# Optimization experiments

Hardware: AMD Instinct MI355X
Metric: run time of the kernel (lower is better)

The kernel has to match this reference:

```python
import jax, jax.numpy as jnp
import numpy as np

N, C, H, T, D, K = 4096, 512, 128, 64, 20, 10


def setup_inputs() -> dict:
    key = jax.random.key(0)
    ks = jax.random.split(key, 40)
    s = 0.05
    inp = {}
    inp["x"] = jax.random.normal(ks[0], (N, D * T), jnp.float32)
    inp["concept_matrix"] = (jax.random.uniform(ks[1], (N, C)) < 0.05).astype(jnp.float32)
    inp["market_value"] = jax.random.uniform(ks[2], (N,), jnp.float32) + 0.1
    # GRU params (torch layout: w_ih [3H,in], w_hh [3H,H], biases [3H]); 2 layers
    inp["gru_w_ih0"] = jax.random.normal(ks[3], (3 * H, D), jnp.float32) * s
    inp["gru_w_hh0"] = jax.random.normal(ks[4], (3 * H, H), jnp.float32) * s
    inp["gru_b_ih0"] = jax.random.normal(ks[5], (3 * H,), jnp.float32) * s
    inp["gru_b_hh0"] = jax.random.normal(ks[6], (3 * H,), jnp.float32) * s
    inp["gru_w_ih1"] = jax.random.normal(ks[7], (3 * H, H), jnp.float32) * s
    inp["gru_w_hh1"] = jax.random.normal(ks[8], (3 * H, H), jnp.float32) * s
    inp["gru_b_ih1"] = jax.random.normal(ks[9], (3 * H,), jnp.float32) * s
    inp["gru_b_hh1"] = jax.random.normal(ks[10], (3 * H,), jnp.float32) * s
    names = ["ps", "hs", "ps_fore", "hs_fore", "ps_back", "hs_back", "indi"]
    for i, n in enumerate(names):
        inp["w_" + n] = jax.random.normal(ks[11 + 2 * i], (H, H), jnp.float32) * s
        inp["b_" + n] = jax.random.normal(ks[12 + 2 * i], (H,), jnp.float32) * s
    inp["w_out"] = jax.random.normal(ks[30], (1, H), jnp.float32) * s
    inp["b_out"] = jax.random.normal(ks[31], (1,), jnp.float32) * s
    return inp


def _cos_sim(x, y):
    # x [n,d], y [m,d] -> [n,m]; NaN (0/0) replaced by 0 via safe denominator
    xy = x @ y.T
    nx = jnp.sqrt(jnp.sum(x * x, axis=1))[:, None]
    ny = jnp.sqrt(jnp.sum(y * y, axis=1))[:, None]
    return xy / jnp.maximum(nx @ ny.T, 1e-12)


def _gru_layer(seq, wih, whh, bih, bhh):
    # seq [T, n, in] -> outputs [T, n, H]
    n = seq.shape[1]
    h0 = jnp.zeros((n, whh.shape[1]), seq.dtype)

    def step(h, xt):
        gx = xt @ wih.T + bih
        gh = h @ whh.T + bhh
        gxr, gxz, gxn = jnp.split(gx, 3, axis=1)
        ghr, ghz, ghn = jnp.split(gh, 3, axis=1)
        r = jax.nn.sigmoid(gxr + ghr)
        z = jax.nn.sigmoid(gxz + ghz)
        ncand = jnp.tanh(gxn + r * ghn)
        hnew = (1.0 - z) * ncand + z * h
        return hnew, hnew

    _, out = jax.lax.scan(step, h0, seq)
    return out


def reference(x, concept_matrix, market_value,
              gru_w_ih0, gru_w_hh0, gru_b_ih0, gru_b_hh0,
              gru_w_ih1, gru_w_hh1, gru_b_ih1, gru_b_hh1,
              w_ps, b_ps, w_hs, b_hs, w_ps_fore, b_ps_fore, w_hs_fore, b_hs_fore,
              w_ps_back, b_ps_back, w_hs_back, b_hs_back, w_indi, b_indi,
              w_out, b_out):
    n = x.shape[0]
    # [n, D*T] -> [n, D, T] -> [n, T, D] -> [T, n, D]
    seq = jnp.swapaxes(x.reshape(n, D, -1).transpose(0, 2, 1), 0, 1)
    out0 = _gru_layer(seq, gru_w_ih0, gru_w_hh0, gru_b_ih0, gru_b_hh0)
    out1 = _gru_layer(out0, gru_w_ih1, gru_w_hh1, gru_b_ih1, gru_b_hh1)
    x_hidden = out1[-1]  # [n, H]

    # --- predefined-concept branch ---
    s2c = concept_matrix * market_value[:, None]
    s2c_den = jnp.sum(s2c, axis=0)[None, :] * concept_matrix + 1.0
    s2c = s2c / s2c_den
    hidden = s2c.T @ x_hidden  # [C, H]
    v1 = jnp.sum(hidden, axis=1) != 0  # valid concepts (replaces row filtering)
    s2c2 = jax.nn.softmax(x_hidden @ hidden.T, axis=0)  # [n, C], column-wise
    hidden2 = s2c2.T @ x_hidden  # [C, H]
    c2s = _cos_sim(x_hidden, hidden2)
    c2s = jax.nn.softmax(jnp.where(v1[None, :], c2s, -1e9), axis=1) * v1[None, :]
    p_shared = c2s @ hidden2
    p_shared = p_shared @ w_ps.T + b_ps
    p_back = p_shared @ w_ps_back.T + b_ps_back
    out_ps = jax.nn.leaky_relu(p_shared @ w_ps_fore.T + b_ps_fore)

    # --- hidden-concept branch ---
    h_shared = x_hidden - p_back
    hs2c = _cos_sim(h_shared, h_shared)  # [n, n]
    diag = jnp.diagonal(hs2c)
    hs2c = hs2c * (1.0 - jnp.eye(n, dtype=hs2c.dtype))
    _, idx = jax.lax.top_k(hs2c, K)  # [n, K]
    mask = jnp.zeros_like(hs2c).at[jnp.arange(n)[:, None], idx].set(1.0)
    hs2c = hs2c * mask
    hs2c = hs2c + jnp.diag((jnp.sum(hs2c, axis=0) != 0).astype(hs2c.dtype) * diag)
    hidden_h = (h_shared.T @ hs2c).T  # [n, H]
    v2 = jnp.sum(hidden_h, axis=1) != 0
    hc2s = _cos_sim(h_shared, hidden_h)
    hc2s = jax.nn.softmax(jnp.where(v2[None, :], hc2s, -1e9), axis=1) * v2[None, :]
    h_si = hc2s @ hidden_h
    h_si = h_si @ w_hs.T + b_hs
    h_back = h_si @ w_hs_back.T + b_hs_back
    out_hs = jax.nn.leaky_relu(h_si @ w_hs_fore.T + b_hs_fore)

    # --- individual branch + head ---
    indi = x_hidden - p_back - h_back
    out_indi = jax.nn.leaky_relu(indi @ w_indi.T + b_indi)
    all_info = out_ps + out_hs + out_indi
    return (all_info @ w_out.T + b_out).squeeze()
```

## Files before the change

kernel.cpp:

```cpp
#include <hip/hip_runtime.h>
#include <cstddef>

#define NR 4096
#define CDIM 512
#define HDIM 128
#define TSTEPS 64
#define DDIM 20
#define KTOP 10

typedef __attribute__((ext_vector_type(8))) short short8;
typedef __attribute__((ext_vector_type(4))) float f32x4;

__device__ __forceinline__ unsigned short f2bf(float f) {
    union { float f; unsigned u; } x; x.f = f;
    unsigned r = (x.u + 0x7fffu + ((x.u >> 16) & 1u)) >> 16;
    return (unsigned short)r;
}
__device__ __forceinline__ unsigned short f2bf_t(float f) {
    union { float f; unsigned u; } x; x.f = f;
    return (unsigned short)(x.u >> 16);
}
__device__ __forceinline__ float bf2f(unsigned short h) {
    union { unsigned u; float f; } x; x.u = ((unsigned)h) << 16;
    return x.f;
}
__device__ __forceinline__ float sigm(float v) {
    return __builtin_amdgcn_rcpf(1.f + __expf(-v));
}
__device__ __forceinline__ float tanh_f(float v) {
    return 1.f - 2.f * __builtin_amdgcn_rcpf(1.f + __expf(2.f * v));
}

#define MFMA16(a, b, c) __builtin_amdgcn_mfma_f32_16x16x32_bf16(a, b, c, 0, 0, 0)

struct MG {
    const float* A; const unsigned short* Bh; const unsigned short* Bl;
    const float* bias; float* C; const float* aux; float* sub;
    const unsigned short* Ah; const unsigned short* Al;
    int N, K, kchunk, flags;
};

__global__ __launch_bounds__(256) void mfma_gemm(MG g)
{
    const int tid = threadIdx.x;
    const int w = tid >> 6, lane = tid & 63, quad = lane >> 4, lm = lane & 15;
    const int bm = (blockIdx.y << 6) + (w << 4);
    const int bn = blockIdx.x << 6;
    const int NC = g.K >> 5;
    const int c0 = (blockIdx.z * g.kchunk) >> 5;
    const int c1 = c0 + (g.kchunk >> 5);
    const float* arow = g.A + (size_t)(bm + lm) * g.K;
    const int packA = g.flags & 16;
    f32x4 acc[4];
    #pragma unroll
    for (int t = 0; t < 4; t++) acc[t] = (f32x4){0.f, 0.f, 0.f, 0.f};

    for (int c = c0; c < c1; c++) {
        short8 ah, al;
        if (packA) {
            size_t aidx = ((size_t)((bm >> 4) * NC + c) * 64 + lane) * 8;
            ah = *(const short8*)(g.Ah + aidx);
            al = *(const short8*)(g.Al + aidx);
        } else {
            const float* ap = arow + (c << 5) + (quad << 3);
            float4 a0 = *(const float4*)ap;
            float4 a1 = *(const float4*)(ap + 4);
            #pragma unroll
            for (int jj = 0; jj < 4; jj++) {
                float f = (&a0.x)[jj];
                unsigned short h = f2bf(f);
                ah[jj] = h; al[jj] = f2bf_t(f - bf2f(h));
                f = (&a1.x)[jj];
                h = f2bf(f);
                ah[4 + jj] = h; al[4 + jj] = f2bf_t(f - bf2f(h));
            }
        }
        #pragma unroll
        for (int t = 0; t < 4; t++) {
            size_t bidx = ((size_t)(((bn >> 4) + t) * NC + c) * 64 + lane) * 8;
            short8 bh = *(const short8*)(g.Bh + bidx);
            short8 bl = *(const short8*)(g.Bl + bidx);
            acc[t] = MFMA16(ah, bh, acc[t]);
            acc[t] = MFMA16(ah, bl, acc[t]);
            acc[t] = MFMA16(al, bh, acc[t]);
        }
    }
    #pragma unroll
    for (int t = 0; t < 4; t++) {
        #pragma unroll
        for (int rg = 0; rg < 4; rg++) {
            int row = bm + (quad << 2) + rg;
            int col = bn + (t << 4) + lm;
            float v = acc[t][rg];
            if (g.flags & 1) v += g.bias[col];
            if (g.flags & 2) v = v > 0.f ? v : 0.01f * v;
            if (g.flags & 4) atomicAdd(&g.C[(size_t)row * g.N + col], v);
            else g.C[(size_t)row * g.N + col] = v;
            if (g.flags & 8)
                g.sub[(size_t)row * g.N + col] = g.aux[(size_t)row * g.N + col] - v;
        }
    }
}

__global__ void pack_bt(const float* __restrict__ src, unsigned short* __restrict__ hi,
                        unsigned short* __restrict__ lo, int K, int total)
{
    int idx = blockIdx.x * 256 + threadIdx.x;
    if (idx >= total) return;
    int NC = K >> 5;
    int lane = idx & 63;
    int c = (idx >> 6) % NC;
    int t = idx / (NC * 64);
    int n = (t << 4) + (lane & 15);
    int kb = (c << 5) + ((lane >> 4) << 3);
    #pragma unroll
    for (int j = 0; j < 8; j++) {
        float f = src[(size_t)n * K + kb + j];
        unsigned short h = f2bf(f);
        hi[(size_t)idx * 8 + j] = h;
        lo[(size_t)idx * 8 + j] = f2bf_t(f - bf2f(h));
    }
}

__global__ void pack_both(const float* __restrict__ src,
                          unsigned short* __restrict__ bth, unsigned short* __restrict__ btl,
                          unsigned short* __restrict__ knh, unsigned short* __restrict__ knl,
                          int N, int total_kn)
{
    int idx = blockIdx.x * 256 + threadIdx.x;
    int lane = idx & 63;
    int totBT = (N >> 4) * 256;
    if (idx < totBT) {
        int c = (idx >> 6) & 3;
        int t = idx >> 8;
        int n = (t << 4) + (lane & 15);
        int kb = (c << 5) + ((lane >> 4) << 3);
        #pragma unroll
        for (int j = 0; j < 8; j++) {
            float f = src[(size_t)n * HDIM + kb + j];
            unsigned short h = f2bf(f);
            bth[(size_t)idx * 8 + j] = h;
            btl[(size_t)idx * 8 + j] = f2bf_t(f - bf2f(h));
        }
    }
    if (idx < total_kn) {
        int NC = N >> 5;
        int c = (idx >> 6) % NC;
        int t = idx / (NC * 64);
        int n = (t << 4) + (lane & 15);
        int kb = (c << 5) + ((lane >> 4) << 3);
        #pragma unroll
        for (int j = 0; j < 8; j++) {
            float f = src[(size_t)(kb + j) * HDIM + n];
            unsigned short h = f2bf(f);
            knh[(size_t)idx * 8 + j] = h;
            knl[(size_t)idx * 8 + j] = f2bf_t(f - bf2f(h));
        }
    }
}

struct W7 {
    const float* src[7];
    unsigned short* hi[7];
    unsigned short* lo[7];
};
__global__ void pack_w7(W7 p)
{
    int idx = blockIdx.x * 256 + threadIdx.x;
    if (idx >= 7 * 2048) return;
    int m = idx >> 11;
    int r = idx & 2047;
    int lane = r & 63;
    int c = (r >> 6) & 3;
    int t = r >> 8;
    int n = (t << 4) + (lane & 15);
    int kb = (c << 5) + ((lane >> 4) << 3);
    const float* src = p.src[m];
    unsigned short* hi = p.hi[m];
    unsigned short* lo = p.lo[m];
    #pragma unroll
    for (int j = 0; j < 8; j++) {
        float f = src[(size_t)n * HDIM + kb + j];
        unsigned short h = f2bf(f);
        hi[(size_t)r * 8 + j] = h;
        lo[(size_t)r * 8 + j] = f2bf_t(f - bf2f(h));
    }
}

__global__ __launch_bounds__(256) void scan_topk(const float* __restrict__ S,
        const float* __restrict__ hn, float* __restrict__ diagv,
        float* __restrict__ tvals, int* __restrict__ tidx)
{
    int row = blockIdx.x;
    const float* d = S + (size_t)row * NR;
    int tid = threadIdx.x;
    int wv = tid >> 6, lane = tid & 63;
    float hi_ = hn[row];
    float lv[16];
    #pragma unroll
    for (int i = 0; i < 16; i++) {
        int j = tid + (i << 8);
        float v = d[j] / fmaxf(hi_ * hn[j], 1e-12f);
        if (j == row) { diagv[row] = v; v = 0.f; }
        lv[i] = v;
    }
    __shared__ float sv[4];
    __shared__ int si[4];
    for (int k = 0; k < KTOP; k++) {
        float bv = -INFINITY; int bi = 0x7fffffff;
        #pragma unroll
        for (int i = 0; i < 16; i++) {
            int j = tid + (i << 8);
            if (lv[i] > bv || (lv[i] == bv && j < bi)) { bv = lv[i]; bi = j; }
        }
        #pragma unroll
        for (int m = 1; m < 64; m <<= 1) {
            float ov = __shfl_xor(bv, m); int oi = __shfl_xor(bi, m);
            if (ov > bv || (ov == bv && oi < bi)) { bv = ov; bi = oi; }
        }
        if (lane == 0) { sv[wv] = bv; si[wv] = bi; }
        __syncthreads();
        bv = sv[0]; bi = si[0];
        #pragma unroll
        for (int w = 1; w < 4; w++) {
            float ov = sv[w]; int oi = si[w];
            if (ov > bv || (ov == bv && oi < bi)) { bv = ov; bi = oi; }
        }
        if (tid == 0) { tvals[row * KTOP + k] = bv; tidx[row * KTOP + k] = bi; }
        if ((bi & 255) == tid) lv[bi >> 8] = -INFINITY;
        __syncthreads();
    }
}

__global__ __launch_bounds__(512) void hc2s_flash(
    const float* __restrict__ hsh, const float* __restrict__ hn,
    const float* __restrict__ hhn, const float* __restrict__ v2,
    const unsigned short* __restrict__ Bh, const unsigned short* __restrict__ Bl,
    const unsigned short* __restrict__ Vh, const unsigned short* __restrict__ Vl,
    float* __restrict__ pO, float* __restrict__ pM, float* __restrict__ pL)
{
    __shared__ __attribute__((aligned(16))) unsigned short Ph[8][16 * 72];
    __shared__ __attribute__((aligned(16))) unsigned short Plo[8][16 * 72];

    const int tid = threadIdx.x;
    const int wv = tid >> 6, lane = tid & 63, quad = lane >> 4, lm = lane & 15;
    const int rg2 = wv >> 1;
    const int cc = wv & 1;
    const int bm = (blockIdx.x << 6) + (rg2 << 4);
    const int rgg = (blockIdx.x << 2) + rg2;
    const int pidx = (blockIdx.y << 1) + cc;
    const int jt0 = (blockIdx.y << 4) + (cc << 3);

    short8 ahh[4], ahl[4];
    #pragma unroll
    for (int c = 0; c < 4; c++) {
        const float* ap = hsh + (size_t)(bm + lm) * HDIM + (c << 5) + (quad << 3);
        float4 a0 = *(const float4*)ap;
        float4 a1 = *(const float4*)(ap + 4);
        #pragma unroll
        for (int j = 0; j < 4; j++) {
            float f = (&a0.x)[j];
            unsigned short h = f2bf(f);
            ahh[c][j] = h; ahl[c][j] = f2bf_t(f - bf2f(h));
            f = (&a1.x)[j];
            h = f2bf(f);
            ahh[c][4 + j] = h; ahl[c][4 + j] = f2bf_t(f - bf2f(h));
        }
    }
    float hnr[4];
    #pragma unroll
    for (int rg = 0; rg < 4; rg++) hnr[rg] = hn[bm + (quad << 2) + rg];

    float m_old[4], l_old[4];
    #pragma unroll
    for (int rg = 0; rg < 4; rg++) { m_old[rg] = -INFINITY; l_old[rg] = 0.f; }
    f32x4 o[8];
    #pragma unroll
    for (int vt = 0; vt < 8; vt++) o[vt] = (f32x4){0.f, 0.f, 0.f, 0.f};

    const int pwr = lm * 72;
    for (int it = 0; it < 8; it++) {
        const int jt = jt0 + it;
        f32x4 s[4];
        #pragma unroll
        for (int tg = 0; tg < 4; tg++) {
            s[tg] = (f32x4){0.f, 0.f, 0.f, 0.f};
            #pragma unroll
            for (int c = 0; c < 4; c++) {
                size_t bidx = ((size_t)(((jt << 2) + tg) * 4 + c) * 64 + lane) * 8;
                short8 bh = *(const short8*)(Bh + bidx);
                short8 bl = *(const short8*)(Bl + bidx);
                s[tg] = MFMA16(ahh[c], bh, s[tg]);
                s[tg] = MFMA16(ahh[c], bl, s[tg]);
                s[tg] = MFMA16(ahl[c], bh, s[tg]);
            }
        }
        float sv[4][4];
        #pragma unroll
        for (int tg = 0; tg < 4; tg++) {
            int col = (jt << 6) + (tg << 4) + lm;
            float hc = hhn[col];
            float vm = v2[col];
            #pragma unroll
            for (int rg = 0; rg < 4; rg++) {
                float v = s[tg][rg] * __builtin_amdgcn_rcpf(fmaxf(hnr[rg] * hc, 1e-12f));
                sv[tg][rg] = (vm == 0.f) ? -1e9f : v;
            }
        }
        float m_new[4], alpha[4], tsum[4], pv[4][4];
        #pragma unroll
        for (int rg = 0; rg < 4; rg++) {
            float m = fmaxf(fmaxf(sv[0][rg], sv[1][rg]), fmaxf(sv[2][rg], sv[3][rg]));
            #pragma unroll
            for (int d = 1; d < 16; d <<= 1) m = fmaxf(m, __shfl_xor(m, d));
            m_new[rg] = fmaxf(m_old[rg], m);
            alpha[rg] = __expf(m_old[rg] - m_new[rg]);
        }
        #pragma unroll
        for (int rg = 0; rg < 4; rg++) {
            float p0_ = __expf(sv[0][rg] - m_new[rg]);
            float p1_ = __expf(sv[1][rg] - m_new[rg]);
            float p2_ = __expf(sv[2][rg] - m_new[rg]);
            float p3_ = __expf(sv[3][rg] - m_new[rg]);
            pv[0][rg] = p0_; pv[1][rg] = p1_; pv[2][rg] = p2_; pv[3][rg] = p3_;
            float ss = p0_ + p1_ + p2_ + p3_;
            #pragma unroll
            for (int d = 1; d < 16; d <<= 1) ss += __shfl_xor(ss, d);
            tsum[rg] = ss;
        }
        #pragma unroll
        for (int rg = 0; rg < 4; rg++) {
            l_old[rg] = l_old[rg] * alpha[rg] + tsum[rg];
            m_old[rg] = m_new[rg];
        }
        #pragma unroll
        for (int vt = 0; vt < 8; vt++) {
            #pragma unroll
            for (int rg = 0; rg < 4; rg++) o[vt][rg] *= alpha[rg];
        }
        #pragma unroll
        for (int tg = 0; tg < 4; tg++) {
            #pragma unroll
            for (int rg = 0; rg < 4; rg++) {
                int off = ((quad << 2) + rg) * 72 + (tg << 4) + lm;
                float p = pv[tg][rg];
                unsigned short h = f2bf(p);
                Ph[wv][off] = h;
                Plo[wv][off] = f2bf_t(p - bf2f(h));
            }
        }
        __asm__ volatile("s_waitcnt lgkmcnt(0)" ::: "memory");
        #pragma unroll
        for (int c2 = 0; c2 < 2; c2++) {
            int poff = pwr + (c2 << 5) + (quad << 3);
            short8 pah = *(const short8*)&Ph[wv][poff];
            short8 pal = *(const short8*)&Plo[wv][poff];
            int cg = (jt << 1) + c2;
            #pragma unroll
            for (int vt = 0; vt < 8; vt++) {
                size_t b0 = ((size_t)(vt * 128 + cg) * 64 + lane) * 8;
                short8 vh = *(const short8*)(Vh + b0);
                short8 vl = *(const short8*)(Vl + b0);
                o[vt] = MFMA16(pah, vh, o[vt]);
                o[vt] = MFMA16(pah, vl, o[vt]);
                o[vt] = MFMA16(pal, vh, o[vt]);
            }
        }
    }
    size_t pb = ((size_t)rgg * 8 + pidx) * 16;
    #pragma unroll
    for (int rg = 0; rg < 4; rg++) {
        int r = (quad << 2) + rg;
        #pragma unroll
        for (int vt = 0; vt < 8; vt++)
            pO[(pb + r) * 128 + (vt << 4) + lm] = o[vt][rg];
    }
    if (lm == 0) {
        #pragma unroll
        for (int rg = 0; rg < 4; rg++) {
            int r = (quad << 2) + rg;
            pM[pb + r] = m_old[rg];
            pL[pb + r] = l_old[rg];
        }
    }
}

__global__ __launch_bounds__(256) void hc2s_merge(const float* __restrict__ pO,
        const float* __restrict__ pM, const float* __restrict__ pL,
        float* __restrict__ O)
{
    int rgg = blockIdx.x;
    int tid = threadIdx.x;
    int r = tid >> 4;
    int c0 = (tid & 15) << 3;
    float m[8], e[8];
    float M = -INFINITY;
    #pragma unroll
    for (int i = 0; i < 8; i++) {
        m[i] = pM[((size_t)rgg * 8 + i) * 16 + r];
        M = fmaxf(M, m[i]);
    }
    float L = 0.f;
    #pragma unroll
    for (int i = 0; i < 8; i++) {
        e[i] = __expf(m[i] - M);
        L += pL[((size_t)rgg * 8 + i) * 16 + r] * e[i];
    }
    float invL = __builtin_amdgcn_rcpf(L);
    float a[8];
    #pragma unroll
    for (int k = 0; k < 8; k++) a[k] = 0.f;
    #pragma unroll
    for (int i = 0; i < 8; i++) {
        const float* src = pO + (((size_t)rgg * 8 + i) * 16 + r) * 128 + c0;
        float4 v0 = *(const float4*)src;
        float4 v1 = *(const float4*)(src + 4);
        a[0] += v0.x * e[i]; a[1] += v0.y * e[i]; a[2] += v0.z * e[i]; a[3] += v0.w * e[i];
        a[4] += v1.x * e[i]; a[5] += v1.y * e[i]; a[6] += v1.z * e[i]; a[7] += v1.w * e[i];
    }
    float* dst = O + ((size_t)rgg * 16 + r) * 128 + c0;
    #pragma unroll
    for (int k = 0; k < 8; k++) dst[k] = a[k] * invL;
}

__global__ void pack_wb(const float* __restrict__ W, unsigned short* __restrict__ Wp,
                        int K, int nch)
{
    int idx = blockIdx.x * 256 + threadIdx.x;
    if (idx >= 24 * nch * 64) return;
    int lane = idx & 63;
    int c = (idx >> 6) % nch;
    int t = idx / (nch * 64);
    int n = t * 16 + (lane & 15);
    int kb = c * 32 + (lane >> 4) * 8;
    #pragma unroll
    for (int j = 0; j < 8; j++) {
        int k = kb + j;
        float f = (k < K) ? W[(size_t)n * K + k] : 0.f;
        Wp[(size_t)idx * 8 + j] = f2bf(f);
    }
}

__global__ __launch_bounds__(512, 2) void gru_mfma(
    const float* __restrict__ xg,
    const unsigned short* __restrict__ wih0p,
    const unsigned short* __restrict__ whh0p,
    const unsigned short* __restrict__ wih1p,
    const unsigned short* __restrict__ whh1p,
    const float* __restrict__ bih0, const float* __restrict__ bhh0,
    const float* __restrict__ bih1, const float* __restrict__ bhh1,
    float* __restrict__ xh)
{
    __shared__ __attribute__((aligned(16))) unsigned short h0A[2][2][16 * 136];
    __shared__ __attribute__((aligned(16))) unsigned short h1A[2][2][16 * 136];
    __shared__ __attribute__((aligned(16))) unsigned short xA[2][2][16 * 40];

    const int tid = threadIdx.x;
    const int w2 = tid >> 6;
    const int lane = tid & 63;
    const int quad = lane >> 4;
    const int lm = lane & 15;
    const int n0 = blockIdx.x << 4;
    const int j = (w2 << 4) + lm;

    for (int i = tid; i < 2 * 2 * 16 * 136; i += 512) {
        ((unsigned short*)h0A)[i] = 0;
        ((unsigned short*)h1A)[i] = 0;
    }
    for (int i = tid; i < 2 * 2 * 16 * 40; i += 512) ((unsigned short*)xA)[i] = 0;

    float br0 = bih0[j] + bhh0[j];
    float bz0 = bih0[128 + j] + bhh0[128 + j];
    float bni0 = bih0[256 + j];
    float bnh0 = bhh0[256 + j];
    float br1 = bih1[j] + bhh1[j];
    float bz1 = bih1[128 + j] + bhh1[128 + j];
    float bni1 = bih1[256 + j];
    float bnh1 = bhh1[256 + j];

    short8 W0x[3], W0h[3][4], W1x[3][4], W1h[3][4];
    {
        const int lb = lane * 8;
        W0x[0] = *(const short8*)&wih0p[(size_t)(w2) * 512 + lb];
        W0x[1] = *(const short8*)&wih0p[(size_t)(8 + w2) * 512 + lb];
        W0x[2] = *(const short8*)&wih0p[(size_t)(16 + w2) * 512 + lb];
        #pragma unroll
        for (int c = 0; c < 4; c++) {
            W0h[0][c] = *(const short8*)&whh0p[(size_t)((w2) * 4 + c) * 512 + lb];
            W0h[1][c] = *(const short8*)&whh0p[(size_t)((8 + w2) * 4 + c) * 512 + lb];
            W0h[2][c] = *(const short8*)&whh0p[(size_t)((16 + w2) * 4 + c) * 512 + lb];
            W1x[0][c] = *(const short8*)&wih1p[(size_t)((w2) * 4 + c) * 512 + lb];
            W1x[1][c] = *(const short8*)&wih1p[(size_t)((8 + w2) * 4 + c) * 512 + lb];
            W1x[2][c] = *(const short8*)&wih1p[(size_t)((16 + w2) * 4 + c) * 512 + lb];
            W1h[0][c] = *(const short8*)&whh1p[(size_t)((w2) * 4 + c) * 512 + lb];
            W1h[1][c] = *(const short8*)&whh1p[(size_t)((8 + w2) * 4 + c) * 512 + lb];
            W1h[2][c] = *(const short8*)&whh1p[(size_t)((16 + w2) * 4 + c) * 512 + lb];
        }
    }

    const int aoff = lm * 136 + quad * 8;
    const int xoff = lm * 40 + quad * 8;
    const bool stager = tid < 16 * DDIM;
    const int sn = tid / DDIM, sd = tid % DDIM;
    const float* xrow = xg + (size_t)(n0 + sn) * (DDIM * TSTEPS) + sd * TSTEPS;
    const int soff = sn * 40 + sd;

    float h0reg[4] = {0.f, 0.f, 0.f, 0.f};
    float h1reg[4] = {0.f, 0.f, 0.f, 0.f};

    if (stager) {
        float v0 = xrow[0], v1 = xrow[1];
        unsigned short a = f2bf_t(v0);
        xA[0][0][soff] = a; xA[0][1][soff] = f2bf_t(v0 - bf2f(a));
        unsigned short b = f2bf_t(v1);
        xA[1][0][soff] = b; xA[1][1][soff] = f2bf_t(v1 - bf2f(b));
    }
    __syncthreads();

    {
        f32x4 accr = (f32x4){br0, br0, br0, br0};
        f32x4 accz = (f32x4){bz0, bz0, bz0, bz0};
        f32x4 accni = (f32x4){bni0, bni0, bni0, bni0};
        short8 axh = *(const short8*)&xA[0][0][xoff];
        short8 axl = *(const short8*)&xA[0][1][xoff];
        accr = MFMA16(axh, W0x[0], accr);
        accr = MFMA16(axl, W0x[0], accr);
        accz = MFMA16(axh, W0x[1], accz);
        accz = MFMA16(axl, W0x[1], accz);
        accni = MFMA16(axh, W0x[2], accni);
        accni = MFMA16(axl, W0x[2], accni);
        #pragma unroll
        for (int rg = 0; rg < 4; rg++) {
            float r = sigm(accr[rg]);
            float z = sigm(accz[rg]);
            float nc = tanh_f(accni[rg] + r * bnh0);
            float hnew = nc - z * nc;
            h0reg[rg] = hnew;
            int off = (quad * 4 + rg) * 136 + j;
            unsigned short hh_ = f2bf_t(hnew);
            h0A[0][0][off] = hh_;
            h0A[0][1][off] = f2bf_t(hnew - bf2f(hh_));
        }
    }
    __syncthreads();

#define GRU_IT(B, DO_L0, XT, LAST)                                                \
{                                                                                 \
    float xv = 0.f;                                                               \
    if ((XT) >= 0 && stager) xv = xrow[XT];          \
    f32x4 accr0 = (f32x4){br0, br0, br0, br0};                                    \
    f32x4 accz0 = (f32x4){bz0, bz0, bz0, bz0};                                    \
    f32x4 accni0 = (f32x4){bni0, bni0, bni0, bni0};                               \
    f32x4 accnh0 = (f32x4){bnh0, bnh0, bnh0, bnh0};                               \
    f32x4 accr1 = (f32x4){br1, br1, br1, br1};                                    \
    f32x4 accz1 = (f32x4){bz1, bz1, bz1, bz1};                                    \
    f32x4 accni1 = (f32x4){bni1, bni1, bni1, bni1};                               \
    f32x4 accnh1 = (f32x4){bnh1, bnh1, bnh1, bnh1};                               \
    if (DO_L0) {                                                                  \
        short8 axh = *(const short8*)&xA[(B) ^ 1][0][xoff];                       \
        short8 axl = *(const short8*)&xA[(B) ^ 1][1][xoff];                       \
        accr0 = MFMA16(axh, W0x[0], accr0);                                       \
        accr0 = MFMA16(axl, W0x[0], accr0);                                       \
        accz0 = MFMA16(axh, W0x[1], accz0);                                       \
        accz0 = MFMA16(axl, W0x[1], accz0);                                       \
        accni0 = MFMA16(axh, W0x[2], accni0);                                     \
        accni0 = MFMA16(axl, W0x[2], accni0);                                     \
    }                                                                             \
    _Pragma("unroll")                                                             \
    for (int c = 0; c < 4; c++) {                                                 \
        short8 a0h = *(const short8*)&h0A[B][0][aoff + c * 32];                   \
        short8 a0l = *(const short8*)&h0A[B][1][aoff + c * 32];                   \
        if (DO_L0) {                                                              \
            accr0 = MFMA16(a0h, W0h[0][c], accr0);                                \
            accr0 = MFMA16(a0l, W0h[0][c], accr0);                                \
            accz0 = MFMA16(a0h, W0h[1][c], accz0);                                \
            accz0 = MFMA16(a0l, W0h[1][c], accz0);                                \
            accnh0 = MFMA16(a0h, W0h[2][c], accnh0);                              \
            accnh0 = MFMA16(a0l, W0h[2][c], accnh0);                              \
        }                                                                         \
        accr1 = MFMA16(a0h, W1x[0][c], accr1);                                    \
        accr1 = MFMA16(a0l, W1x[0][c], accr1);                                    \
        accz1 = MFMA16(a0h, W1x[1][c], accz1);                                    \
        accz1 = MFMA16(a0l, W1x[1][c], accz1);                                    \
        accni1 = MFMA16(a0h, W1x[2][c], accni1);                                  \
        accni1 = MFMA16(a0l, W1x[2][c], accni1);                                  \
        short8 a1h = *(const short8*)&h1A[(B) ^ 1][0][aoff + c * 32];             \
        short8 a1l = *(const short8*)&h1A[(B) ^ 1][1][aoff + c * 32];             \
        accr1 = MFMA16(a1h, W1h[0][c], accr1);                                    \
        accr1 = MFMA16(a1l, W1h[0][c], accr1);                                    \
        accz1 = MFMA16(a1h, W1h[1][c], accz1);                                    \
        accz1 = MFMA16(a1l, W1h[1][c], accz1);                                    \
        accnh1 = MFMA16(a1h, W1h[2][c], accnh1);                                  \
        accnh1 = MFMA16(a1l, W1h[2][c], accnh1);                                  \
    }                                                                             \
    if (DO_L0) {                                                                  \
        _Pragma("unroll")                                                         \
        for (int rg = 0; rg < 4; rg++) {                                          \
            float r = sigm(accr0[rg]);                                            \
            float z = sigm(accz0[rg]);                                            \
            float nc = tanh_f(accni0[rg] + r * accnh0[rg]);                       \
            float hnew = nc + z * (h0reg[rg] - nc);                               \
            h0reg[rg] = hnew;                                                     \
            int off = (quad * 4 + rg) * 136 + j;                                  \
            unsigned short hh_ = f2bf_t(hnew);                                    \
            h0A[(B) ^ 1][0][off] = hh_;                                           \
            h0A[(B) ^ 1][1][off] = f2bf_t(hnew - bf2f(hh_));                      \
        }                                                                         \
    }                                                                             \
    _Pragma("unroll")                                                             \
    for (int rg = 0; rg < 4; rg++) {                                              \
        float r = sigm(accr1[rg]);                                                \
        float z = sigm(accz1[rg]);                                                \
        float nc = tanh_f(accni1[rg] + r * accnh1[rg]);                           \
        float hnew = nc + z * (h1reg[rg] - nc);                                   \
        h1reg[rg] = hnew;                                                         \
        if (LAST) {                                                               \
            xh[(size_t)(n0 + quad * 4 + rg) * HDIM + j] = hnew;                   \
        } else {                                                                  \
            int off = (quad * 4 + rg) * 136 + j;                                  \
            unsigned short hh_ = f2bf_t(hnew);                                    \
            h1A[B][0][off] = hh_;                                                 \
            h1A[B][1][off] = f2bf_t(hnew - bf2f(hh_));                            \
        }                                                                         \
    }                                                                             \
    if ((XT) >= 0 && stager) {                                                    \
        unsigned short hh_ = f2bf_t(xv);                                          \
        xA[B][0][soff] = hh_;                                                     \
        xA[B][1][soff] = f2bf_t(xv - bf2f(hh_));                                  \
    }                                                                             \
    if (!(LAST)) __syncthreads();                                                 \
}

    for (int i = 0; i < 62; i += 2) {
        GRU_IT(0, true, i + 2, false)
        GRU_IT(1, true, i + 3, false)
    }
    GRU_IT(0, true, -1, false)
    GRU_IT(1, false, -1, true)
#undef GRU_IT
}

__global__ __launch_bounds__(256) void den_atomic(const float* __restrict__ cm,
        const float* __restrict__ mv, float* __restrict__ den)
{
    int c = blockIdx.x * 64 + (threadIdx.x & 63);
    int rg = threadIdx.x >> 6;
    int nbase = blockIdx.y * 128;
    float acc = 0.f;
    for (int i = 0; i < 32; i++) {
        int n = nbase + rg + (i << 2);
        acc += cm[(size_t)n * CDIM + c] * mv[n];
    }
    __shared__ float red[4][64];
    red[rg][threadIdx.x & 63] = acc;
    __syncthreads();
    if (rg == 0)
        atomicAdd(&den[c], red[0][threadIdx.x] + red[1][threadIdx.x] +
                           red[2][threadIdx.x] + red[3][threadIdx.x]);
}

__global__ __launch_bounds__(256) void s2ct_trans(const float* __restrict__ cm,
        const float* __restrict__ mv, const float* __restrict__ den,
        float* __restrict__ s2cT)
{
    __shared__ float tile[64][65];
    __shared__ float mvs[64];
    const int tid = threadIdx.x;
    const int n0 = blockIdx.x << 6;
    const int c0 = blockIdx.y << 6;
    const int lc = tid & 63, lr = tid >> 6;
    if (tid < 64) mvs[tid] = mv[n0 + tid];
    #pragma unroll
    for (int i = 0; i < 16; i++) {
        int n = lr + (i << 2);
        tile[n][lc] = cm[(size_t)(n0 + n) * CDIM + c0 + lc];
    }
    __syncthreads();
    #pragma unroll
    for (int i = 0; i < 16; i++) {
        int c = lr + (i << 2);
        float m = tile[lc][c];
        float d = den[c0 + c];
        s2cT[(size_t)(c0 + c) * NR + n0 + lc] = (m * mvs[lc]) / (d * m + 1.f);
    }
}

__global__ void row_norm(const float* __restrict__ a, float* __restrict__ out)
{
    int r = blockIdx.x;
    float acc = 0.f;
    for (int h = threadIdx.x; h < HDIM; h += 64) {
        float v = a[(size_t)r * HDIM + h];
        acc += v * v;
    }
    for (int o = 32; o > 0; o >>= 1) acc += __shfl_down(acc, o);
    if (threadIdx.x == 0) out[r] = sqrtf(acc);
}

__global__ void row_nonzero(const float* __restrict__ a, float* __restrict__ out)
{
    int r = blockIdx.x;
    float acc = 0.f;
    for (int h = threadIdx.x; h < HDIM; h += 64) acc += a[(size_t)r * HDIM + h];
    for (int o = 32; o > 0; o >>= 1) acc += __shfl_down(acc, o);
    if (threadIdx.x == 0) out[r] = (acc != 0.f) ? 1.f : 0.f;
}

__global__ void row_norm_nz(const float* __restrict__ a, float* __restrict__ nrm,
                            float* __restrict__ nz)
{
    int r = blockIdx.x;
    float acc = 0.f, s = 0.f;
    for (int h = threadIdx.x; h < HDIM; h += 64) {
        float v = a[(size_t)r * HDIM + h];
        acc += v * v;
        s += v;
    }
    for (int o = 32; o > 0; o >>= 1) { acc += __shfl_down(acc, o); s += __shfl_down(s, o); }
    if (threadIdx.x == 0) { nrm[r] = sqrtf(acc); nz[r] = (s != 0.f) ? 1.f : 0.f; }
}

__global__ __launch_bounds__(256) void cos_softmax_row(float* __restrict__ data, int N,
        const float* __restrict__ rn, const float* __restrict__ cn,
        const float* __restrict__ vmask)
{
    int row = blockIdx.x;
    float* d = data + (size_t)row * N;
    int tid = threadIdx.x;
    int wv = tid >> 6, lane = tid & 63;
    __shared__ float red[8];
    float rnv = rn ? rn[row] : 0.f;
    float mx = -INFINITY;
    for (int j = tid; j < N; j += 256) {
        float v = d[j];
        if (cn) v = v * __builtin_amdgcn_rcpf(fmaxf(rnv * cn[j], 1e-12f));
        if (vmask && vmask[j] == 0.f) v = -1e9f;
        d[j] = v;
        mx = fmaxf(mx, v);
    }
    #pragma unroll
    for (int m = 1; m < 64; m <<= 1) mx = fmaxf(mx, __shfl_xor(mx, m));
    if (lane == 0) red[wv] = mx;
    __syncthreads();
    float M = fmaxf(fmaxf(red[0], red[1]), fmaxf(red[2], red[3]));
    float sum = 0.f;
    for (int j = tid; j < N; j += 256) {
        float e = __expf(d[j] - M);
        d[j] = e;
        sum += e;
    }
    #pragma unroll
    for (int m = 1; m < 64; m <<= 1) sum += __shfl_xor(sum, m);
    if (lane == 0) red[4 + wv] = sum;
    __syncthreads();
    float inv = __builtin_amdgcn_rcpf(red[4] + red[5] + red[6] + red[7]);
    for (int j = tid; j < N; j += 256) {
        float v = d[j] * inv;
        if (vmask) v *= vmask[j];
        d[j] = v;
    }
}

__global__ void colsum_scatter(const float* __restrict__ vals, const int* __restrict__ idxs,
                               float* __restrict__ colsum)
{
    int idx = blockIdx.x * 256 + threadIdx.x;
    if (idx < NR * KTOP) atomicAdd(&colsum[idxs[idx]], vals[idx]);
}

__global__ void hh_scatter(const float* __restrict__ vals, const int* __restrict__ idxs,
                           const float* __restrict__ hsh, float* __restrict__ hh)
{
    int p = blockIdx.x;
    int j = idxs[p];
    float v = vals[p];
    int i = p / KTOP;
    atomicAdd(&hh[(size_t)j * HDIM + threadIdx.x], v * hsh[(size_t)i * HDIM + threadIdx.x]);
}

__global__ void hh_diag(const float* __restrict__ colsum, const float* __restrict__ diag,
                        const float* __restrict__ hsh, float* __restrict__ hh)
{
    int idx = blockIdx.x * 256 + threadIdx.x;
    int j = idx >> 7;
    if (colsum[j] != 0.f) hh[idx] += diag[j] * hsh[idx];
}

__global__ void head_kernel(const float* __restrict__ ps, const float* __restrict__ hs,
                            const float* __restrict__ indi, const float* __restrict__ w,
                            const float* __restrict__ b, float* __restrict__ out)
{
    int n = blockIdx.x;
    int t = threadIdx.x;
    float acc = 0.f;
    for (int h = t; h < HDIM; h += 64) {
        size_t k = (size_t)n * HDIM + h;
        acc += (ps[k] + hs[k] + indi[k]) * w[h];
    }
    for (int o = 32; o > 0; o >>= 1) acc += __shfl_down(acc, o);
    if (t == 0) out[n] = acc + b[0];
}

static inline void mg(hipStream_t s, const float* A, const unsigned short* Bh,
                      const unsigned short* Bl, const float* bias, float* C,
                      int M, int N, int K, int z, int flags,
                      const float* aux = nullptr, float* sub = nullptr,
                      const unsigned short* Ah = nullptr, const unsigned short* Al = nullptr)
{
    MG g{A, Bh, Bl, bias, C, aux, sub, Ah, Al, N, K, K / z,
         flags | (z > 1 ? 4 : 0) | (Ah ? 16 : 0)};
    mfma_gemm<<<dim3(N / 64, M / 64, z), 256, 0, s>>>(g);
}
static inline void pbt(hipStream_t s, const float* src, unsigned short* hi,
                       unsigned short* lo, int N, int K)
{
    int total = (N / 16) * (K / 32) * 64;
    pack_bt<<<(total + 255) / 256, 256, 0, s>>>(src, hi, lo, K, total);
}
static inline void pboth(hipStream_t s, const float* src,
                         unsigned short* bth, unsigned short* btl,
                         unsigned short* knh, unsigned short* knl, int N)
{
    int totBT = (N / 16) * 4 * 64;
    int totKN = 8 * (N / 32) * 64;
    int tot = totBT > totKN ? totBT : totKN;
    pack_both<<<(tot + 255) / 256, 256, 0, s>>>(src, bth, btl, knh, knl, N, totKN);
}

extern "C" void kernel_launch(void* const* d_in, const int* in_sizes, int n_in,
                              void* d_out, int out_size, void* d_ws, size_t ws_size,
                              hipStream_t stream)
{
    (void)in_sizes; (void)n_in; (void)out_size; (void)ws_size;
    const float* x    = (const float*)d_in[0];
    const float* cm   = (const float*)d_in[1];
    const float* mv   = (const float*)d_in[2];
    const float* wih0 = (const float*)d_in[3];
    const float* whh0 = (const float*)d_in[4];
    const float* bih0 = (const float*)d_in[5];
    const float* bhh0 = (const float*)d_in[6];
    const float* wih1 = (const float*)d_in[7];
    const float* whh1 = (const float*)d_in[8];
    const float* bih1 = (const float*)d_in[9];
    const float* bhh1 = (const float*)d_in[10];
    const float* w_ps = (const float*)d_in[11];
    const float* b_ps = (const float*)d_in[12];
    const float* w_hs = (const float*)d_in[13];
    const float* b_hs = (const float*)d_in[14];
    const float* w_ps_fore = (const float*)d_in[15];
    const float* b_ps_fore = (const float*)d_in[16];
    const float* w_hs_fore = (const float*)d_in[17];
    const float* b_hs_fore = (const float*)d_in[18];
    const float* w_ps_back = (const float*)d_in[19];
    const float* b_ps_back = (const float*)d_in[20];
    const float* w_hs_back = (const float*)d_in[21];
    const float* b_hs_back = (const float*)d_in[22];
    const float* w_indi = (const float*)d_in[23];
    const float* b_indi = (const float*)d_in[24];
    const float* w_out  = (const float*)d_in[25];
    const float* b_out  = (const float*)d_in[26];
    float* out = (float*)d_out;

    float* ws = (float*)d_ws;
    float* BIG = ws;
    float* h0 = ws + 16777216;
    float* h1 = h0 + 524288;
    float* den = h1 + 524288;
    float* v1 = den + 512;
    float* hidden = v1 + 512;
    float* hidden2 = hidden + 65536;
    float* xnorm = hidden2 + 65536;
    float* h2n = xnorm + 4096;
    float* p0 = h2n + 512;
    float* p_shared = p0 + 524288;
    float* p_back = p_shared + 524288;
    float* out_ps = p_back + 524288;
    float* h_shared = out_ps + 524288;
    float* hn = h_shared + 524288;
    float* diagv = hn + 4096;
    float* colsum = diagv + 4096;
    float* tvals = colsum + 4096;
    int*   tidx = (int*)(tvals + 40960);
    float* hidden_h = (float*)(tidx + 40960);
    float* v2 = hidden_h + 524288;
    float* hhn = v2 + 4096;
    float* hsi0 = hhn + 4096;
    float* h_si = hsi0 + 524288;
    float* h_back = h_si + 524288;
    float* out_hs = h_back + 524288;
    float* indi = out_hs + 524288;
    float* out_indi = indi + 524288;
    float* extra = out_indi + 524288;

    unsigned short* wih0p = (unsigned short*)(BIG + 5242880);
    unsigned short* whh0p = wih0p + 12288;
    unsigned short* wih1p = whh0p + 49152;
    unsigned short* whh1p = wih1p + 49152;
    float* s2cT = BIG;
    float* L    = BIG + 2097152;
    float* c2s  = BIG + 4194304;
    unsigned short* PB = (unsigned short*)(BIG + 6291456);
    unsigned short* pbt_xh_hi = PB;
    unsigned short* pbt_xh_lo = pbt_xh_hi + 524288;
    unsigned short* pkn_xh_hi = pbt_xh_lo + 524288;
    unsigned short* pkn_xh_lo = pkn_xh_hi + 524288;
    unsigned short* pbt_h2_hi = pkn_xh_lo + 524288;
    unsigned short* pbt_h2_lo = pbt_h2_hi + 65536;
    unsigned short* pkn_h2_hi = pbt_h2_lo + 65536;
    unsigned short* pkn_h2_lo = pkn_h2_hi + 65536;
    unsigned short* wps_hi  = pkn_h2_lo + 65536;
    unsigned short* wps_lo  = wps_hi + 16384;
    unsigned short* wpsb_hi = wps_lo + 16384;
    unsigned short* wpsb_lo = wpsb_hi + 16384;
    unsigned short* wpsf_hi = wpsb_lo + 16384;
    unsigned short* wpsf_lo = wpsf_hi + 16384;
    unsigned short* pbt_hsh_hi = (unsigned short*)p0;
    unsigned short* pbt_hsh_lo = pbt_hsh_hi + 524288;
    unsigned short* pbt_hh_hi = (unsigned short*)indi;
    unsigned short* pbt_hh_lo = pbt_hh_hi + 524288;
    unsigned short* pkn_hh_hi = (unsigned short*)out_indi;
    unsigned short* pkn_hh_lo = pkn_hh_hi + 524288;
    float* part_O = BIG;
    float* part_m = BIG + 4194304;
    float* part_l = BIG + 4227072;
    unsigned short* EX = (unsigned short*)extra;
    unsigned short* whs_hi  = EX;            unsigned short* whs_lo  = EX + 16384;
    unsigned short* whsb_hi = EX + 32768;    unsigned short* whsb_lo = EX + 49152;
    unsigned short* whsf_hi = EX + 65536;    unsigned short* whsf_lo = EX + 81920;
    unsigned short* wind_hi = EX + 98304;    unsigned short* wind_lo = EX + 114688;

    pack_wb<<<6, 256, 0, stream>>>(wih0, wih0p, DDIM, 1);
    pack_wb<<<24, 256, 0, stream>>>(whh0, whh0p, HDIM, 4);
    pack_wb<<<24, 256, 0, stream>>>(wih1, wih1p, HDIM, 4);
    pack_wb<<<24, 256, 0, stream>>>(whh1, whh1p, HDIM, 4);
    {
        W7 w7;
        w7.src[0] = w_ps;      w7.hi[0] = wps_hi;  w7.lo[0] = wps_lo;
        w7.src[1] = w_ps_back; w7.hi[1] = wpsb_hi; w7.lo[1] = wpsb_lo;
        w7.src[2] = w_ps_fore; w7.hi[2] = wpsf_hi; w7.lo[2] = wpsf_lo;
        w7.src[3] = w_hs;      w7.hi[3] = whs_hi;  w7.lo[3] = whs_lo;
        w7.src[4] = w_hs_back; w7.hi[4] = whsb_hi; w7.lo[4] = whsb_lo;
        w7.src[5] = w_hs_fore; w7.hi[5] = whsf_hi; w7.lo[5] = whsf_lo;
        w7.src[6] = w_indi;    w7.hi[6] = wind_hi; w7.lo[6] = wind_lo;
        pack_w7<<<56, 256, 0, stream>>>(w7);
    }
    gru_mfma<<<NR / 16, 512, 0, stream>>>(x, wih0p, whh0p, wih1p, whh1p,
                                          bih0, bhh0, bih1, bhh1, h1);
    float* x_hidden = h1;

    hipMemsetAsync(den, 0, CDIM * sizeof(float), stream);
    den_atomic<<<dim3(CDIM / 64, 32), 256, 0, stream>>>(cm, mv, den);
    s2ct_trans<<<dim3(NR / 64, CDIM / 64), 256, 0, stream>>>(cm, mv, den, s2cT);
    pboth(stream, x_hidden, pbt_xh_hi, pbt_xh_lo, pkn_xh_hi, pkn_xh_lo, NR);
    hipMemsetAsync(hidden, 0, 65536 * sizeof(float), stream);
    mg(stream, s2cT, pkn_xh_hi, pkn_xh_lo, nullptr, hidden, CDIM, HDIM, NR, 8, 0);
    row_nonzero<<<CDIM, 64, 0, stream>>>(hidden, v1);
    mg(stream, hidden, pbt_xh_hi, pbt_xh_lo, nullptr, L, CDIM, NR, HDIM, 1, 0);
    cos_softmax_row<<<CDIM, 256, 0, stream>>>(L, NR, nullptr, nullptr, nullptr);
    hipMemsetAsync(hidden2, 0, 65536 * sizeof(float), stream);
    mg(stream, L, pkn_xh_hi, pkn_xh_lo, nullptr, hidden2, CDIM, HDIM, NR, 8, 0);
    row_norm<<<NR, 64, 0, stream>>>(x_hidden, xnorm);
    row_norm<<<CDIM, 64, 0, stream>>>(hidden2, h2n);
    pboth(stream, hidden2, pbt_h2_hi, pbt_h2_lo, pkn_h2_hi, pkn_h2_lo, CDIM);
    mg(stream, x_hidden, pbt_h2_hi, pbt_h2_lo, nullptr, c2s, NR, CDIM, HDIM, 1, 0,
       nullptr, nullptr, pbt_xh_hi, pbt_xh_lo);
    cos_softmax_row<<<NR, 256, 0, stream>>>(c2s, CDIM, xnorm, h2n, v1);
    hipMemsetAsync(p0, 0, 524288 * sizeof(float), stream);
    mg(stream, c2s, pkn_h2_hi, pkn_h2_lo, nullptr, p0, NR, HDIM, CDIM, 2, 0);
    mg(stream, p0, wps_hi, wps_lo, b_ps, p_shared, NR, HDIM, HDIM, 1, 1);
    mg(stream, p_shared, wpsb_hi, wpsb_lo, b_ps_back, p_back, NR, HDIM, HDIM, 1, 1 | 8,
       x_hidden, h_shared);
    mg(stream, p_shared, wpsf_hi, wpsf_lo, b_ps_fore, out_ps, NR, HDIM, HDIM, 1, 1 | 2);

    row_norm<<<NR, 64, 0, stream>>>(h_shared, hn);
    pbt(stream, h_shared, pbt_hsh_hi, pbt_hsh_lo, NR, HDIM);
    mg(stream, h_shared, pbt_hsh_hi, pbt_hsh_lo, nullptr, BIG, NR, NR, HDIM, 1, 0,
       nullptr, nullptr, pbt_hsh_hi, pbt_hsh_lo);
    scan_topk<<<NR, 256, 0, stream>>>(BIG, hn, diagv, tvals, tidx);
    hipMemsetAsync(colsum, 0, NR * sizeof(float), stream);
    hipMemsetAsync(hidden_h, 0, 524288 * sizeof(float), stream);
    colsum_scatter<<<(NR * KTOP + 255) / 256, 256, 0, stream>>>(tvals, tidx, colsum);
    hh_scatter<<<NR * KTOP, HDIM, 0, stream>>>(tvals, tidx, h_shared, hidden_h);
    hh_diag<<<2048, 256, 0, stream>>>(colsum, diagv, h_shared, hidden_h);
    row_norm_nz<<<NR, 64, 0, stream>>>(hidden_h, hhn, v2);
    pboth(stream, hidden_h, pbt_hh_hi, pbt_hh_lo, pkn_hh_hi, pkn_hh_lo, NR);
    hc2s_flash<<<dim3(NR / 64, 4), 512, 0, stream>>>(h_shared, hn, hhn, v2,
                                                     pbt_hh_hi, pbt_hh_lo,
                                                     pkn_hh_hi, pkn_hh_lo,
                                                     part_O, part_m, part_l);
    hc2s_merge<<<NR / 16, 256, 0, stream>>>(part_O, part_m, part_l, hsi0);
    mg(stream, hsi0, whs_hi, whs_lo, b_hs, h_si, NR, HDIM, HDIM, 1, 1);
    mg(stream, h_si, whsb_hi, whsb_lo, b_hs_back, h_back, NR, HDIM, HDIM, 1, 1 | 8,
       h_shared, indi);
    mg(stream, h_si, whsf_hi, whsf_lo, b_hs_fore, out_hs, NR, HDIM, HDIM, 1, 1 | 2);

    mg(stream, indi, wind_hi, wind_lo, b_indi, out_indi, NR, HDIM, HDIM, 1, 1 | 2);
    head_kernel<<<NR, 64, 0, stream>>>(out_ps, out_hs, out_indi, w_out, b_out, out);
}
```

Baseline: 749.6 us.

## Fuse output head into GEMM epilogues, merge dual GEMMs, consolidate memsets and scatters

The separate head kernel is removed. The fore-branch GEMMs now accumulate leaky_relu(x)·w_out directly into the output through atomics, so the out_ps, out_hs and out_indi intermediates are never stored. Each back/fore GEMM pair sharing an A operand is launched once using blockIdx.z as a selector. The scattered zeroing memsets become one contiguous memset, colsum_scatter is merged into a per-row hh_scatter, and split-K factors are doubled. This trades fewer launches and less memory traffic for more atomics on the output and on split-K accumulations.

```diff
diff --git a/kernel.cpp b/kernel.cpp
--- a/kernel.cpp
+++ b/kernel.cpp
@@ -37,7 +37,10 @@
     const float* A; const unsigned short* Bh; const unsigned short* Bl;
     const float* bias; float* C; const float* aux; float* sub;
     const unsigned short* Ah; const unsigned short* Al;
-    int N, K, kchunk, flags;
+    const unsigned short* Bh2; const unsigned short* Bl2;
+    const float* bias2; float* C2;
+    const float* wout; const float* bout; float* hout;
+    int N, K, kchunk, flags, flags2;
 };
 
 __global__ __launch_bounds__(256) void mfma_gemm(MG g)
@@ -47,7 +50,17 @@
     const int bm = (blockIdx.y << 6) + (w << 4);
     const int bn = blockIdx.x << 6;
     const int NC = g.K >> 5;
-    const int c0 = (blockIdx.z * g.kchunk) >> 5;
+    int flags = g.flags;
+    const unsigned short* Bh = g.Bh;
+    const unsigned short* Bl = g.Bl;
+    const float* bias = g.bias;
+    float* C = g.C;
+    int zk = blockIdx.z;
+    if (g.flags & 32) {
+        if (blockIdx.z) { Bh = g.Bh2; Bl = g.Bl2; bias = g.bias2; C = g.C2; flags = g.flags2; }
+        zk = 0;
+    }
+    const int c0 = (zk * g.kchunk) >> 5;
     const int c1 = c0 + (g.kchunk >> 5);
     const float* arow = g.A + (size_t)(bm + lm) * g.K;
     const int packA = g.flags & 16;
@@ -78,13 +91,14 @@
         #pragma unroll
         for (int t = 0; t < 4; t++) {
             size_t bidx = ((size_t)(((bn >> 4) + t) * NC + c) * 64 + lane) * 8;
-            short8 bh = *(const short8*)(g.Bh + bidx);
-            short8 bl = *(const short8*)(g.Bl + bidx);
+            short8 bh = *(const short8*)(Bh + bidx);
+            short8 bl = *(const short8*)(Bl + bidx);
             acc[t] = MFMA16(ah, bh, acc[t]);
             acc[t] = MFMA16(ah, bl, acc[t]);
             acc[t] = MFMA16(al, bh, acc[t]);
         }
     }
+    float rsum[4] = {0.f, 0.f, 0.f, 0.f};
     #pragma unroll
     for (int t = 0; t < 4; t++) {
         #pragma unroll
@@ -92,12 +106,30 @@
             int row = bm + (quad << 2) + rg;
             int col = bn + (t << 4) + lm;
             float v = acc[t][rg];
-            if (g.flags & 1) v += g.bias[col];
-            if (g.flags & 2) v = v > 0.f ? v : 0.01f * v;
-            if (g.flags & 4) atomicAdd(&g.C[(size_t)row * g.N + col], v);
-            else g.C[(size_t)row * g.N + col] = v;
-            if (g.flags & 8)
+            if (flags & 1) v += bias[col];
+            if (flags & 2) v = v > 0.f ? v : 0.01f * v;
+            if (flags & 64) rsum[rg] += v * g.wout[col];
+            if (!(flags & 128)) {
+                if (flags & 4) atomicAdd(&C[(size_t)row * g.N + col], v);
+                else C[(size_t)row * g.N + col] = v;
+            }
+            if (flags & 8)
                 g.sub[(size_t)row * g.N + col] = g.aux[(size_t)row * g.N + col] - v;
+        }
+    }
+    if (flags & 64) {
+        #pragma unroll
+        for (int rg = 0; rg < 4; rg++) {
+            #pragma unroll
+            for (int d = 1; d < 16; d <<= 1) rsum[rg] += __shfl_xor(rsum[rg], d);
+        }
+        if (lm == 0) {
+            #pragma unroll
+            for (int rg = 0; rg < 4; rg++) {
+                float s = rsum[rg];
+                if ((flags & 256) && bn == 0) s += g.bout[0];
+                atomicAdd(&g.hout[bm + (quad << 2) + rg], s);
+            }
         }
     }
 }
@@ -761,21 +793,24 @@
     }
 }
 
-__global__ void colsum_scatter(const float* __restrict__ vals, const int* __restrict__ idxs,
-                               float* __restrict__ colsum)
-{
-    int idx = blockIdx.x * 256 + threadIdx.x;
-    if (idx < NR * KTOP) atomicAdd(&colsum[idxs[idx]], vals[idx]);
-}
-
 __global__ void hh_scatter(const float* __restrict__ vals, const int* __restrict__ idxs,
-                           const float* __restrict__ hsh, float* __restrict__ hh)
-{
-    int p = blockIdx.x;
-    int j = idxs[p];
-    float v = vals[p];
-    int i = p / KTOP;
-    atomicAdd(&hh[(size_t)j * HDIM + threadIdx.x], v * hsh[(size_t)i * HDIM + threadIdx.x]);
+                           const float* __restrict__ hsh, float* __restrict__ hh,
+                           float* __restrict__ colsum)
+{
+    int i = blockIdx.x;
+    int t = threadIdx.x;
+    float hv = hsh[(size_t)i * HDIM + t];
+    #pragma unroll
+    for (int k = 0; k < KTOP; k++) {
+        int p = i * KTOP + k;
+        int jj = idxs[p];
+        float v = vals[p];
+        atomicAdd(&hh[(size_t)jj * HDIM + t], v * hv);
+    }
+    if (t < KTOP) {
+        int p = i * KTOP + t;
+        atomicAdd(&colsum[idxs[p]], vals[p]);
+    }
 }
 
 __global__ void hh_diag(const float* __restrict__ colsum, const float* __restrict__ diag,
@@ -784,32 +819,34 @@
     int idx = blockIdx.x * 256 + threadIdx.x;
     int j = idx >> 7;
     if (colsum[j] != 0.f) hh[idx] += diag[j] * hsh[idx];
-}
-
-__global__ void head_kernel(const float* __restrict__ ps, const float* __restrict__ hs,
-                            const float* __restrict__ indi, const float* __restrict__ w,
-                            const float* __restrict__ b, float* __restrict__ out)
-{
-    int n = blockIdx.x;
-    int t = threadIdx.x;
-    float acc = 0.f;
-    for (int h = t; h < HDIM; h += 64) {
-        size_t k = (size_t)n * HDIM + h;
-        acc += (ps[k] + hs[k] + indi[k]) * w[h];
-    }
-    for (int o = 32; o > 0; o >>= 1) acc += __shfl_down(acc, o);
-    if (t == 0) out[n] = acc + b[0];
 }
 
 static inline void mg(hipStream_t s, const float* A, const unsigned short* Bh,
                       const unsigned short* Bl, const float* bias, float* C,
                       int M, int N, int K, int z, int flags,
                       const float* aux = nullptr, float* sub = nullptr,
-                      const unsigned short* Ah = nullptr, const unsigned short* Al = nullptr)
-{
-    MG g{A, Bh, Bl, bias, C, aux, sub, Ah, Al, N, K, K / z,
-         flags | (z > 1 ? 4 : 0) | (Ah ? 16 : 0)};
+                      const unsigned short* Ah = nullptr, const unsigned short* Al = nullptr,
+                      const float* wout = nullptr, const float* bout = nullptr,
+                      float* hout = nullptr)
+{
+    MG g{A, Bh, Bl, bias, C, aux, sub, Ah, Al,
+         nullptr, nullptr, nullptr, nullptr, wout, bout, hout,
+         N, K, K / z, flags | (z > 1 ? 4 : 0) | (Ah ? 16 : 0), 0};
     mfma_gemm<<<dim3(N / 64, M / 64, z), 256, 0, s>>>(g);
+}
+static inline void mg_dual(hipStream_t s, const float* A,
+                           const unsigned short* Bh, const unsigned short* Bl,
+                           const float* bias, float* C, int flags1,
+                           const unsigned short* Bh2, const unsigned short* Bl2,
+                           const float* bias2, float* C2, int flags2,
+                           int M, int N, int K,
+                           const float* aux, float* sub,
+                           const float* wout, const float* bout, float* hout)
+{
+    MG g{A, Bh, Bl, bias, C, aux, sub, nullptr, nullptr,
+         Bh2, Bl2, bias2, C2, wout, bout, hout,
+         N, K, K, flags1 | 32, flags2};
+    mfma_gemm<<<dim3(N / 64, M / 64, 2), 256, 0, s>>>(g);
 }
 static inline void pbt(hipStream_t s, const float* src, unsigned short* hi,
                        unsigned short* lo, int N, int K)
@@ -863,34 +900,32 @@
 
     float* ws = (float*)d_ws;
     float* BIG = ws;
-    float* h0 = ws + 16777216;
-    float* h1 = h0 + 524288;
-    float* den = h1 + 524288;
-    float* v1 = den + 512;
-    float* hidden = v1 + 512;
-    float* hidden2 = hidden + 65536;
-    float* xnorm = hidden2 + 65536;
+    float* zero0 = ws + 16777216;
+    float* den      = zero0;
+    float* hidden   = den + 512;
+    float* hidden2  = hidden + 65536;
+    float* colsum   = hidden2 + 65536;
+    float* p0       = colsum + 4096;
+    float* hidden_h = p0 + 524288;
+    const size_t ZERO_FLOATS = 512 + 65536 + 65536 + 4096 + 524288 + 524288;
+    float* h1 = hidden_h + 524288;
+    float* v1 = h1 + 524288;
+    float* xnorm = v1 + 512;
     float* h2n = xnorm + 4096;
-    float* p0 = h2n + 512;
-    float* p_shared = p0 + 524288;
+    float* p_shared = h2n + 512;
     float* p_back = p_shared + 524288;
-    float* out_ps = p_back + 524288;
-    float* h_shared = out_ps + 524288;
+    float* h_shared = p_back + 524288;
     float* hn = h_shared + 524288;
     float* diagv = hn + 4096;
-    float* colsum = diagv + 4096;
-    float* tvals = colsum + 4096;
+    float* tvals = diagv + 4096;
     int*   tidx = (int*)(tvals + 40960);
-    float* hidden_h = (float*)(tidx + 40960);
-    float* v2 = hidden_h + 524288;
+    float* v2 = (float*)(tidx + 40960);
     float* hhn = v2 + 4096;
     float* hsi0 = hhn + 4096;
     float* h_si = hsi0 + 524288;
     float* h_back = h_si + 524288;
-    float* out_hs = h_back + 524288;
-    float* indi = out_hs + 524288;
-    float* out_indi = indi + 524288;
-    float* extra = out_indi + 524288;
+    float* indi = h_back + 524288;
+    float* extra = indi + 524288;
 
     unsigned short* wih0p = (unsigned short*)(BIG + 5242880);
     unsigned short* whh0p = wih0p + 12288;
@@ -918,7 +953,7 @@
     unsigned short* pbt_hsh_lo = pbt_hsh_hi + 524288;
     unsigned short* pbt_hh_hi = (unsigned short*)indi;
     unsigned short* pbt_hh_lo = pbt_hh_hi + 524288;
-    unsigned short* pkn_hh_hi = (unsigned short*)out_indi;
+    unsigned short* pkn_hh_hi = (unsigned short*)hsi0;
     unsigned short* pkn_hh_lo = pkn_hh_hi + 524288;
     float* part_O = BIG;
     float* part_m = BIG + 4194304;
@@ -928,6 +963,9 @@
     unsigned short* whsb_hi = EX + 32768;    unsigned short* whsb_lo = EX + 49152;
     unsigned short* whsf_hi = EX + 65536;    unsigned short* whsf_lo = EX + 81920;
     unsigned short* wind_hi = EX + 98304;    unsigned short* wind_lo = EX + 114688;
+
+    hipMemsetAsync(zero0, 0, ZERO_FLOATS * sizeof(float), stream);
+    hipMemsetAsync(out, 0, NR * sizeof(float), stream);
 
     pack_wb<<<6, 256, 0, stream>>>(wih0, wih0p, DDIM, 1);
     pack_wb<<<24, 256, 0, stream>>>(whh0, whh0p, HDIM, 4);
@@ -948,39 +986,33 @@
                                           bih0, bhh0, bih1, bhh1, h1);
     float* x_hidden = h1;
 
-    hipMemsetAsync(den, 0, CDIM * sizeof(float), stream);
     den_atomic<<<dim3(CDIM / 64, 32), 256, 0, stream>>>(cm, mv, den);
     s2ct_trans<<<dim3(NR / 64, CDIM / 64), 256, 0, stream>>>(cm, mv, den, s2cT);
     pboth(stream, x_hidden, pbt_xh_hi, pbt_xh_lo, pkn_xh_hi, pkn_xh_lo, NR);
-    hipMemsetAsync(hidden, 0, 65536 * sizeof(float), stream);
-    mg(stream, s2cT, pkn_xh_hi, pkn_xh_lo, nullptr, hidden, CDIM, HDIM, NR, 8, 0);
+    mg(stream, s2cT, pkn_xh_hi, pkn_xh_lo, nullptr, hidden, CDIM, HDIM, NR, 16, 0);
     row_nonzero<<<CDIM, 64, 0, stream>>>(hidden, v1);
     mg(stream, hidden, pbt_xh_hi, pbt_xh_lo, nullptr, L, CDIM, NR, HDIM, 1, 0);
     cos_softmax_row<<<CDIM, 256, 0, stream>>>(L, NR, nullptr, nullptr, nullptr);
-    hipMemsetAsync(hidden2, 0, 65536 * sizeof(float), stream);
-    mg(stream, L, pkn_xh_hi, pkn_xh_lo, nullptr, hidden2, CDIM, HDIM, NR, 8, 0);
+    mg(stream, L, pkn_xh_hi, pkn_xh_lo, nullptr, hidden2, CDIM, HDIM, NR, 16, 0);
     row_norm<<<NR, 64, 0, stream>>>(x_hidden, xnorm);
     row_norm<<<CDIM, 64, 0, stream>>>(hidden2, h2n);
     pboth(stream, hidden2, pbt_h2_hi, pbt_h2_lo, pkn_h2_hi, pkn_h2_lo, CDIM);
     mg(stream, x_hidden, pbt_h2_hi, pbt_h2_lo, nullptr, c2s, NR, CDIM, HDIM, 1, 0,
        nullptr, nullptr, pbt_xh_hi, pbt_xh_lo);
     cos_softmax_row<<<NR, 256, 0, stream>>>(c2s, CDIM, xnorm, h2n, v1);
-    hipMemsetAsync(p0, 0, 524288 * sizeof(float), stream);
-    mg(stream, c2s, pkn_h2_hi, pkn_h2_lo, nullptr, p0, NR, HDIM, CDIM, 2, 0);
+    mg(stream, c2s, pkn_h2_hi, pkn_h2_lo, nullptr, p0, NR, HDIM, CDIM, 4, 0);
     mg(stream, p0, wps_hi, wps_lo, b_ps, p_shared, NR, HDIM, HDIM, 1, 1);
-    mg(stream, p_shared, wpsb_hi, wpsb_lo, b_ps_back, p_back, NR, HDIM, HDIM, 1, 1 | 8,
-       x_hidden, h_shared);
-    mg(stream, p_shared, wpsf_hi, wpsf_lo, b_ps_fore, out_ps, NR, HDIM, HDIM, 1, 1 | 2);
+    mg_dual(stream, p_shared,
+            wpsb_hi, wpsb_lo, b_ps_back, p_back, 1 | 8,
+            wpsf_hi, wpsf_lo, b_ps_fore, nullptr, 1 | 2 | 64 | 128,
+            NR, HDIM, HDIM, x_hidden, h_shared, w_out, b_out, out);
 
     row_norm<<<NR, 64, 0, stream>>>(h_shared, hn);
     pbt(stream, h_shared, pbt_hsh_hi, pbt_hsh_lo, NR, HDIM);
     mg(stream, h_shared, pbt_hsh_hi, pbt_hsh_lo, nullptr, BIG, NR, NR, HDIM, 1, 0,
        nullptr, nullptr, pbt_hsh_hi, pbt_hsh_lo);
     scan_topk<<<NR, 256, 0, stream>>>(BIG, hn, diagv, tvals, tidx);
-    hipMemsetAsync(colsum, 0, NR * sizeof(float), stream);
-    hipMemsetAsync(hidden_h, 0, 524288 * sizeof(float), stream);
-    colsum_scatter<<<(NR * KTOP + 255) / 256, 256, 0, stream>>>(tvals, tidx, colsum);
-    hh_scatter<<<NR * KTOP, HDIM, 0, stream>>>(tvals, tidx, h_shared, hidden_h);
+    hh_scatter<<<NR, HDIM, 0, stream>>>(tvals, tidx, h_shared, hidden_h, colsum);
     hh_diag<<<2048, 256, 0, stream>>>(colsum, diagv, h_shared, hidden_h);
     row_norm_nz<<<NR, 64, 0, stream>>>(hidden_h, hhn, v2);
     pboth(stream, hidden_h, pbt_hh_hi, pbt_hh_lo, pkn_hh_hi, pkn_hh_lo, NR);
@@ -990,10 +1022,12 @@
                                                      part_O, part_m, part_l);
     hc2s_merge<<<NR / 16, 256, 0, stream>>>(part_O, part_m, part_l, hsi0);
     mg(stream, hsi0, whs_hi, whs_lo, b_hs, h_si, NR, HDIM, HDIM, 1, 1);
-    mg(stream, h_si, whsb_hi, whsb_lo, b_hs_back, h_back, NR, HDIM, HDIM, 1, 1 | 8,
-       h_shared, indi);
-    mg(stream, h_si, whsf_hi, whsf_lo, b_hs_fore, out_hs, NR, HDIM, HDIM, 1, 1 | 2);
-
-    mg(stream, indi, wind_hi, wind_lo, b_indi, out_indi, NR, HDIM, HDIM, 1, 1 | 2);
-    head_kernel<<<NR, 64, 0, stream>>>(out_ps, out_hs, out_indi, w_out, b_out, out);
-}
+    mg_dual(stream, h_si,
+            whsb_hi, whsb_lo, b_hs_back, h_back, 1 | 8,
+            whsf_hi, whsf_lo, b_hs_fore, nullptr, 1 | 2 | 64 | 128,
+            NR, HDIM, HDIM, h_shared, indi, w_out, b_out, out);
+
+    mg(stream, indi, wind_hi, wind_lo, b_indi, nullptr, NR, HDIM, HDIM, 1,
+       1 | 2 | 64 | 128 | 256, nullptr, nullptr, nullptr, nullptr,
+       w_out, b_out, out);
+}
```

Result: faster. 697.1 us (-7.0%).
